# Kernel optimization log

Hardware: AMD Instinct MI355X
Metric: run time of the kernel (lower is better)

Reference implementation:

```python
import jax, jax.numpy as jnp
import numpy as np

N, E, G = 100000, 1600000, 8
IN, H, OUT = 3, 64, 20


def setup_inputs() -> dict:
    key = jax.random.key(0)
    ks = jax.random.split(key, 24)
    def nrm(k, shape, scale=0.1):
        return jax.random.normal(k, shape, dtype=jnp.float32) * scale
    inp = {}
    inp["x"] = jax.random.normal(ks[0], (N, IN), dtype=jnp.float32)
    inp["edge_index"] = jax.random.randint(ks[1], (2, E), 0, N, dtype=jnp.int32)
    inp["batch"] = jnp.sort(jax.random.randint(ks[2], (N,), 0, G, dtype=jnp.int32))
    dims = [(IN, H), (H, H), (H, H)]  # 3 GATConv layers (initial + layers-1)
    for i, (di, do) in enumerate(dims):
        inp[f"W{i}"] = nrm(ks[3 + 4 * i], (di, do))
        inp[f"as{i}"] = nrm(ks[4 + 4 * i], (do,))
        inp[f"ad{i}"] = nrm(ks[5 + 4 * i], (do,))
        inp[f"b{i}"] = jnp.zeros((do,), jnp.float32)
    inp["vn_emb0"] = jnp.zeros((1, H), jnp.float32)  # constant-0 init per module
    inp["m1_w1"] = nrm(ks[15], (H, H)); inp["m1_b1"] = jnp.zeros((H,), jnp.float32)
    inp["m1_w2"] = nrm(ks[16], (H, H)); inp["m1_b2"] = jnp.zeros((H,), jnp.float32)
    inp["mf_w1"] = nrm(ks[17], (H, H)); inp["mf_b1"] = jnp.zeros((H,), jnp.float32)
    inp["mf_w2"] = nrm(ks[18], (H, OUT)); inp["mf_b2"] = jnp.zeros((OUT,), jnp.float32)
    inp["out_w"] = nrm(ks[19], (H, OUT)); inp["out_b"] = jnp.zeros((OUT,), jnp.float32)
    return inp


def _gat(x, src, dst, W, a_s, a_d, b):
    # PyG GATConv, 1 head: h = xW; e_ij = LeakyReLU_0.2(a_s.h_j + a_d.h_i);
    # alpha = softmax over incoming edges of each dst node; out_i = sum_j alpha_ij h_j + b
    h = x @ W                                                  # [N, H]
    lg = jax.nn.leaky_relu((h @ a_s)[src] + (h @ a_d)[dst], 0.2)  # [E+N]
    m = jax.ops.segment_max(lg, dst, num_segments=N)
    m = jnp.where(jnp.isfinite(m), m, 0.0)
    p = jnp.exp(lg - m[dst])
    denom = jax.ops.segment_sum(p, dst, num_segments=N)
    alpha = p / denom[dst]
    return jax.ops.segment_sum(alpha[:, None] * h[src], dst, num_segments=N) + b


def _forward(x, edge_index, batch, params):
    (W0, as0, ad0, b0, W1, as1, ad1, b1, W2, as2, ad2, b2,
     vn_emb0, m1_w1, m1_b1, m1_w2, m1_b2, mf_w1, mf_b1, mf_w2, mf_b2,
     out_w, out_b) = params
    loops = jnp.arange(N, dtype=edge_index.dtype)  # GATConv add_self_loops=True
    src = jnp.concatenate([edge_index[0], loops])
    dst = jnp.concatenate([edge_index[1], loops])
    act = lambda v: jax.nn.leaky_relu(v, 0.01)  # nn.LeakyReLU default slope
    h = act(_gat(x, src, dst, W0, as0, ad0, b0))
    h = act(_gat(h, src, dst, W1, as1, ad1, b1))
    h = act(_gat(h, src, dst, W2, as2, ad2, b2))
    # virtual node: global_add_pool(out, batch) + Embedding(0) (zero-init)
    vn = jax.ops.segment_sum(h, batch, num_segments=G) + vn_emb0[0]
    vn = jax.nn.relu(vn @ m1_w1 + m1_b1)
    vn = jax.nn.relu(vn @ m1_w2 + m1_b2)
    vn = jax.nn.relu(vn @ mf_w1 + mf_b1)
    vn = jax.nn.relu(vn @ mf_w2 + mf_b2)
    return (h @ out_w + out_b, vn)


def reference(x, edge_index, batch, W0, as0, ad0, b0, W1, as1, ad1, b1,
              W2, as2, ad2, b2, vn_emb0, m1_w1, m1_b1, m1_w2, m1_b2,
              mf_w1, mf_b1, mf_w2, mf_b2, out_w, out_b):
    params = (W0, as0, ad0, b0, W1, as1, ad1, b1, W2, as2, ad2, b2,
              vn_emb0, m1_w1, m1_b1, m1_w2, m1_b2, mf_w1, mf_b1, mf_w2, mf_b2,
              out_w, out_b)
    return _forward(x, edge_index, batch, params)
```

## Files before the change

kernel.cpp:

```cpp
#include <hip/hip_runtime.h>
#include <hip/hip_bf16.h>

#define H 64
#define OUTD 20
#define NGRAPH 8
#define CAP 64
#define NBK 256
#define CAPB 8192

typedef __attribute__((ext_vector_type(8))) short bf16x8;
typedef __attribute__((ext_vector_type(4))) float f32x4;
typedef __attribute__((ext_vector_type(8))) unsigned short u16x8;

__device__ __forceinline__ float ldp(const void* p, int i, bool f32) {
    return f32 ? ((const float*)p)[i]
               : __bfloat162float(((const __hip_bfloat16*)p)[i]);
}

__device__ __forceinline__ float bfu(unsigned short u) {
    union { unsigned int i; float f; } c; c.i = ((unsigned)u) << 16; return c.f;
}
__device__ __forceinline__ unsigned short fbits(float f) {
    __hip_bfloat16 b = __float2bfloat16(f);
    return *reinterpret_cast<unsigned short*>(&b);
}

__global__ void detect_dtype(const unsigned short* __restrict__ xb, int n_u16,
                             int* __restrict__ flag) {
    __shared__ int sh[256];
    int t = threadIdx.x;
    int m = min(n_u16, 4096);
    int bad = 0;
    for (int i = t; i < m; i += 256) {
        unsigned e = (xb[i] >> 7) & 0xFF;
        bad += (e >= 0x90) ? 1 : 0;
    }
    sh[t] = bad;
    __syncthreads();
    for (int off = 128; off; off >>= 1) {
        if (t < off) sh[t] += sh[t + off];
        __syncthreads();
    }
    if (t == 0) *flag = (sh[0] > (m >> 4)) ? 1 : 0;
}


__global__ void fillC_dense0(const int* __restrict__ src, const int* __restrict__ dst,
                             int* __restrict__ gcur, unsigned* __restrict__ ebuf,
                             int E, int n, int nC, int EPC, int nbk,
                             const void* __restrict__ x, const void* __restrict__ W,
                             const void* __restrict__ a_s, const void* __restrict__ a_d,
                             __hip_bfloat16* __restrict__ h, float* __restrict__ s,
                             float* __restrict__ d, const int* __restrict__ flagp) {
    if ((int)blockIdx.x < nC) {
        __shared__ unsigned lcnt[NBK];
        __shared__ int lbase[NBK];
        int t = threadIdx.x;
        for (int i = t; i < NBK; i += 256) lcnt[i] = 0;
        __syncthreads();
        int base = blockIdx.x * (256 * EPC) + t;
        for (int i = 0; i < EPC; ++i) {
            int e = base + i * 256;
            if (e < E) {
                int dn = dst[e];
                if ((unsigned)dn < (unsigned)n) atomicAdd(&lcnt[dn >> 9], 1u);
            }
        }
        __syncthreads();
        for (int i = t; i < nbk; i += 256) {
            unsigned c = lcnt[i];
            lbase[i] = c ? atomicAdd(&gcur[i], (int)c) : 0;
            lcnt[i] = 0;
        }
        __syncthreads();
        for (int i = 0; i < EPC; ++i) {
            int e = base + i * 256;
            if (e < E) {
                int dn = dst[e];
                if ((unsigned)dn < (unsigned)n) {
                    int b = dn >> 9;
                    unsigned pos = (unsigned)lbase[b] + atomicAdd(&lcnt[b], 1u);
                    if (pos < CAPB)
                        ebuf[(size_t)b * CAPB + pos] =
                            ((unsigned)src[e] << 9) | (unsigned)(dn & 511);
                }
            }
        }
        return;
    }
    const bool f32 = (*flagp != 0);
    int idx = ((int)blockIdx.x - nC) * 256 + threadIdx.x;
    int node = idx >> 6;
    int f = idx & 63;
    if (node >= n) return;
    float acc = 0.f;
    for (int k = 0; k < 3; ++k)
        acc += ldp(x, node * 3 + k, f32) * ldp(W, k * H + f, f32);
    h[(size_t)node * H + f] = __float2bfloat16(acc);
    float sv = acc * ldp(a_s, f, f32);
    float dv = acc * ldp(a_d, f, f32);
    for (int off = 32; off; off >>= 1) {
        sv += __shfl_xor(sv, off);
        dv += __shfl_xor(dv, off);
    }
    if (f == 0) { s[node] = sv; d[node] = dv; }
}

__global__ __launch_bounds__(512) void bucketD(const unsigned* __restrict__ ebuf,
                                               const int* __restrict__ gcur,
                                               int* __restrict__ cnt,
                                               int* __restrict__ col, int n) {
    __shared__ unsigned lcnt[512];
    int b = blockIdx.x, t = threadIdx.x;
    lcnt[t] = 0;
    __syncthreads();
    int end = min(gcur[b], CAPB);
    const unsigned* reg = ebuf + (size_t)b * CAPB;
    for (int i = t; i < end; i += 512) {
        unsigned e = reg[i];
        int loc = (int)(e & 511u);
        int sn = (int)(e >> 9);
        unsigned pos = atomicAdd(&lcnt[loc], 1u);
        if (pos < CAP) col[(size_t)((b << 9) + loc) * CAP + pos] = sn;
    }
    __syncthreads();
    int node = (b << 9) + t;
    if (node < n) cnt[node] = (int)min(lcnt[t], (unsigned)CAP);
}


__global__ __launch_bounds__(256) void denseN_mfma(
    const __hip_bfloat16* __restrict__ in,
    const void* __restrict__ W,
    const void* __restrict__ a_s, const void* __restrict__ a_d,
    __hip_bfloat16* __restrict__ h, float* __restrict__ s,
    float* __restrict__ d, int n, const int* __restrict__ flagp) {
    const bool f32 = (*flagp != 0);
    __shared__ short Wt[64 * 72];
    int t = threadIdx.x;
    for (int i = t; i < 4096; i += 256) {
        int k = i >> 6, nf = i & 63;
        Wt[nf * 72 + k] = (short)fbits(ldp(W, i, f32));
    }
    __syncthreads();

    int wid = t >> 6, lane = t & 63;
    int quad = lane >> 4, n16 = lane & 15;
    int nodeBase = blockIdx.x * 64 + wid * 16;
    int mrow = nodeBase + n16;
    int mclamp = min(mrow, n - 1);
    const short* inp = (const short*)in;
    const short* arow = inp + (size_t)mclamp * 64;
    bf16x8 a0 = *(const bf16x8*)(arow + quad * 8);
    bf16x8 a1 = *(const bf16x8*)(arow + 32 + quad * 8);

    float as_v[4], ad_v[4];
    for (int nt = 0; nt < 4; ++nt) {
        as_v[nt] = ldp(a_s, nt * 16 + n16, f32);
        ad_v[nt] = ldp(a_d, nt * 16 + n16, f32);
    }

    float sv[4] = {0.f, 0.f, 0.f, 0.f}, dv[4] = {0.f, 0.f, 0.f, 0.f};
    f32x4 accs[4];
    for (int nt = 0; nt < 4; ++nt) {
        const short* wrow = Wt + (nt * 16 + n16) * 72;
        bf16x8 b0 = *(const bf16x8*)(wrow + quad * 8);
        bf16x8 b1 = *(const bf16x8*)(wrow + 32 + quad * 8);
        f32x4 c = {0.f, 0.f, 0.f, 0.f};
        c = __builtin_amdgcn_mfma_f32_16x16x32_bf16(a0, b0, c, 0, 0, 0);
        c = __builtin_amdgcn_mfma_f32_16x16x32_bf16(a1, b1, c, 0, 0, 0);
        accs[nt] = c;
        for (int r = 0; r < 4; ++r) {
            sv[r] += c[r] * as_v[nt];
            dv[r] += c[r] * ad_v[nt];
        }
    }

    for (int r = 0; r < 4; ++r) {
        int node = nodeBase + quad * 4 + r;
        if (node < n) {
            __hip_bfloat16* hr = h + (size_t)node * 64;
            for (int nt = 0; nt < 4; ++nt)
                hr[nt * 16 + n16] = __float2bfloat16(accs[nt][r]);
        }
    }
    for (int r = 0; r < 4; ++r) {
        for (int mask = 1; mask < 16; mask <<= 1) {
            sv[r] += __shfl_xor(sv[r], mask);
            dv[r] += __shfl_xor(dv[r], mask);
        }
    }
    if (n16 == 0) {
        for (int r = 0; r < 4; ++r) {
            int node = nodeBase + quad * 4 + r;
            if (node < n) { s[node] = sv[r]; d[node] = dv[r]; }
        }
    }
}


__global__ void gat_aggregate(const __hip_bfloat16* __restrict__ h,
                              const float* __restrict__ s, const float* __restrict__ d,
                              const int* __restrict__ cnt, const int* __restrict__ col,
                              const void* __restrict__ bias,
                              __hip_bfloat16* __restrict__ out, int n,
                              const int* __restrict__ flagp) {
    const bool f32 = (*flagp != 0);
    int node = (blockIdx.x * blockDim.x + threadIdx.x) >> 6;
    if (node >= n) return;
    int lane = threadIdx.x & 63;
    int deg = min(cnt[node], CAP);
    int D = deg + 1;
    size_t base = (size_t)node * CAP;
    float di = d[node];

    if (D <= 64) {
        bool act = lane < D;
        int j = (lane < deg) ? col[base + lane] : node;
        j = ((unsigned)j < (unsigned)n) ? j : 0;
        float v = act ? s[j] + di : -INFINITY;
        v = v > 0.f ? v : 0.2f * v;
        float m = v;
        for (int off = 32; off; off >>= 1) m = fmaxf(m, __shfl_xor(m, off));
        float wgt = act ? __expf(v - m) : 0.f;
        float wsum = wgt;
        for (int off = 32; off; off >>= 1) wsum += __shfl_xor(wsum, off);

        const u16x8* h8 = (const u16x8*)h;
        int c = lane & 7, q = lane >> 3;
        float a[8] = {0.f, 0.f, 0.f, 0.f, 0.f, 0.f, 0.f, 0.f};
        int groups = (D + 7) >> 3;
        for (int p = 0; p < groups; ++p) {
            int t = 8 * p + q;
            float wt = __shfl(wgt, t);
            int jt = __shfl(j, t);
            u16x8 hv = h8[jt * 8 + c];
            a[0] += wt * bfu(hv[0]);
            a[1] += wt * bfu(hv[1]);
            a[2] += wt * bfu(hv[2]);
            a[3] += wt * bfu(hv[3]);
            a[4] += wt * bfu(hv[4]);
            a[5] += wt * bfu(hv[5]);
            a[6] += wt * bfu(hv[6]);
            a[7] += wt * bfu(hv[7]);
        }
        for (int i = 0; i < 8; ++i) {
            a[i] += __shfl_xor(a[i], 8);
            a[i] += __shfl_xor(a[i], 16);
            a[i] += __shfl_xor(a[i], 32);
        }
        if (lane < 8) {
            float inv = 1.f / fmaxf(wsum, 1e-20f);
            u16x8 ov;
            for (int i = 0; i < 8; ++i) {
                float o = a[i] * inv + ldp(bias, 8 * c + i, f32);
                o = o > 0.f ? o : 0.01f * o;
                ov[i] = fbits(o);
            }
            ((u16x8*)out)[(size_t)node * 8 + c] = ov;
        }
        return;
    }

    float m = -INFINITY;
    for (int e = lane; e < D; e += 64) {
        int j = (e < deg) ? col[base + e] : node;
        j = ((unsigned)j < (unsigned)n) ? j : 0;
        float v = s[j] + di;
        v = v > 0.f ? v : 0.2f * v;
        m = fmaxf(m, v);
    }
    for (int off = 32; off; off >>= 1) m = fmaxf(m, __shfl_xor(m, off));
    if (!(m > -INFINITY)) m = 0.f;

    float acc = 0.f, wsum = 0.f;
    for (int b = 0; b < D; b += 64) {
        int e = b + lane;
        float w = 0.f;
        int j = 0;
        if (e < D) {
            j = (e < deg) ? col[base + e] : node;
            j = ((unsigned)j < (unsigned)n) ? j : 0;
            float v = s[j] + di;
            v = v > 0.f ? v : 0.2f * v;
            w = __expf(v - m);
        }
        wsum += w;
        int c2 = min(64, D - b);
        for (int t = 0; t < c2; ++t) {
            float wt = __shfl(w, t);
            int jt = __shfl(j, t);
            acc += wt * __bfloat162float(h[(size_t)jt * H + lane]);
        }
    }
    for (int off = 32; off; off >>= 1) wsum += __shfl_xor(wsum, off);

    float o = acc / fmaxf(wsum, 1e-20f) + ldp(bias, lane, f32);
    o = o > 0.f ? o : 0.01f * o;
    out[(size_t)node * H + lane] = __float2bfloat16(o);
}


__global__ __launch_bounds__(256) void proj_pool(
    const __hip_bfloat16* __restrict__ h,
    const void* __restrict__ W, const void* __restrict__ b,
    void* __restrict__ out, int n, const int* __restrict__ flagp,
    int projBlocks, const int* __restrict__ batch, float* __restrict__ vn) {
    const bool f32 = (*flagp != 0);
    if ((int)blockIdx.x < projBlocks) {
        __shared__ short Wt[32 * 72];
        int t = threadIdx.x;
        for (int i = t; i < 32 * 64; i += 256) {
            int o = i >> 6, k = i & 63;
            Wt[o * 72 + k] = (o < OUTD) ? (short)fbits(ldp(W, k * OUTD + o, f32)) : 0;
        }
        __syncthreads();

        int wid = t >> 6, lane = t & 63;
        int quad = lane >> 4, n16 = lane & 15;
        int nodeBase = blockIdx.x * 64 + wid * 16;
        int mclamp = min(nodeBase + n16, n - 1);
        const short* arow = (const short*)h + (size_t)mclamp * 64;
        bf16x8 a0 = *(const bf16x8*)(arow + quad * 8);
        bf16x8 a1 = *(const bf16x8*)(arow + 32 + quad * 8);

        f32x4 acc0 = {0.f, 0.f, 0.f, 0.f}, acc1 = {0.f, 0.f, 0.f, 0.f};
        {
            const short* wrow = Wt + n16 * 72;
            bf16x8 b0 = *(const bf16x8*)(wrow + quad * 8);
            bf16x8 b1 = *(const bf16x8*)(wrow + 32 + quad * 8);
            acc0 = __builtin_amdgcn_mfma_f32_16x16x32_bf16(a0, b0, acc0, 0, 0, 0);
            acc0 = __builtin_amdgcn_mfma_f32_16x16x32_bf16(a1, b1, acc0, 0, 0, 0);
        }
        {
            const short* wrow = Wt + (16 + n16) * 72;
            bf16x8 b0 = *(const bf16x8*)(wrow + quad * 8);
            bf16x8 b1 = *(const bf16x8*)(wrow + 32 + quad * 8);
            acc1 = __builtin_amdgcn_mfma_f32_16x16x32_bf16(a0, b0, acc1, 0, 0, 0);
            acc1 = __builtin_amdgcn_mfma_f32_16x16x32_bf16(a1, b1, acc1, 0, 0, 0);
        }
        float bv0 = ldp(b, n16, f32);
        float bv1 = (n16 < OUTD - 16) ? ldp(b, 16 + n16, f32) : 0.f;
        for (int r = 0; r < 4; ++r) {
            int node = nodeBase + quad * 4 + r;
            if (node >= n) break;
            float o0 = acc0[r] + bv0;
            if (f32) ((float*)out)[node * OUTD + n16] = o0;
            else     ((__hip_bfloat16*)out)[node * OUTD + n16] = __float2bfloat16(o0);
            if (n16 < OUTD - 16) {
                float o1 = acc1[r] + bv1;
                if (f32) ((float*)out)[node * OUTD + 16 + n16] = o1;
                else     ((__hip_bfloat16*)out)[node * OUTD + 16 + n16] = __float2bfloat16(o1);
            }
        }
        return;
    }
    __shared__ float part[NGRAPH * H];
    int t = threadIdx.x;
    for (int i = t; i < NGRAPH * H; i += 256) part[i] = 0.f;
    __syncthreads();
    int pb = (int)blockIdx.x - projBlocks;
    int npb = gridDim.x - projBlocks;
    int wid = t >> 6, lane = t & 63;
    int gwave = pb * 4 + wid;
    int nwaves = npb * 4;
    int chunk = (n + nwaves - 1) / nwaves;
    int beg = gwave * chunk;
    int end = min(n, beg + chunk);
    if (beg < end) {
        float acc = 0.f;
        int cur = batch[beg];
        for (int i = beg; i < end; ++i) {
            int g = batch[i];
            if (g != cur) {
                if ((unsigned)cur < NGRAPH) atomicAdd(&part[cur * H + lane], acc);
                acc = 0.f;
                cur = g;
            }
            acc += __bfloat162float(h[(size_t)i * H + lane]);
        }
        if ((unsigned)cur < NGRAPH) atomicAdd(&part[cur * H + lane], acc);
    }
    __syncthreads();
    for (int i = t; i < NGRAPH * H; i += 256) {
        float v = part[i];
        if (v != 0.f) atomicAdd(&vn[i], v);
    }
}


__global__ void vn_mlp(const float* __restrict__ vn, const void* __restrict__ emb,
                       const void* __restrict__ w1, const void* __restrict__ b1,
                       const void* __restrict__ w2, const void* __restrict__ b2,
                       const void* __restrict__ w3, const void* __restrict__ b3,
                       const void* __restrict__ w4, const void* __restrict__ b4,
                       void* __restrict__ out, int out1_off, const int* __restrict__ flagp) {
    const bool f32 = (*flagp != 0);
    __shared__ float A[NGRAPH * H], B[NGRAPH * H];
    int t = threadIdx.x;
    int g = t >> 6, f = t & 63;
    A[t] = vn[t] + ldp(emb, f, f32);
    __syncthreads();
    float acc = ldp(b1, f, f32);
    for (int k = 0; k < H; ++k) acc += A[g * H + k] * ldp(w1, k * H + f, f32);
    B[t] = fmaxf(acc, 0.f);
    __syncthreads();
    acc = ldp(b2, f, f32);
    for (int k = 0; k < H; ++k) acc += B[g * H + k] * ldp(w2, k * H + f, f32);
    A[t] = fmaxf(acc, 0.f);
    __syncthreads();
    acc = ldp(b3, f, f32);
    for (int k = 0; k < H; ++k) acc += A[g * H + k] * ldp(w3, k * H + f, f32);
    B[t] = fmaxf(acc, 0.f);
    __syncthreads();
    if (f < OUTD) {
        acc = ldp(b4, f, f32);
        for (int k = 0; k < H; ++k) acc += B[g * H + k] * ldp(w4, k * OUTD + f, f32);
        acc = fmaxf(acc, 0.f);
        int idx = out1_off + g * OUTD + f;
        if (f32) ((float*)out)[idx] = acc;
        else     ((__hip_bfloat16*)out)[idx] = __float2bfloat16(acc);
    }
}


extern "C" void kernel_launch(void* const* d_in, const int* in_sizes, int n_in,
                              void* d_out, int out_size, void* d_ws, size_t ws_size,
                              hipStream_t stream) {
    const void* x   = d_in[0];
    const int* ei   = (const int*)d_in[1];
    const int* batch= (const int*)d_in[2];
    const void* W0  = d_in[3];
    const void* as0 = d_in[4];
    const void* ad0 = d_in[5];
    const void* b0  = d_in[6];
    const void* W1  = d_in[7];
    const void* as1 = d_in[8];
    const void* ad1 = d_in[9];
    const void* b1  = d_in[10];
    const void* W2  = d_in[11];
    const void* as2 = d_in[12];
    const void* ad2 = d_in[13];
    const void* b2  = d_in[14];
    const void* vne = d_in[15];
    const void* m1w1 = d_in[16];
    const void* m1b1 = d_in[17];
    const void* m1w2 = d_in[18];
    const void* m1b2 = d_in[19];
    const void* mfw1 = d_in[20];
    const void* mfb1 = d_in[21];
    const void* mfw2 = d_in[22];
    const void* mfb2 = d_in[23];
    const void* outw = d_in[24];
    const void* outb = d_in[25];

    const int N = in_sizes[2];
    const int E = in_sizes[1] / 2;
    const int* srcp = ei;
    const int* dstp = ei + E;

    char* w = (char*)d_ws;
    auto alloc = [&](size_t bytes) -> void* {
        void* p = (void*)w;
        w += ((bytes + 255) / 256) * 256;
        return p;
    };
    int*   flag   = (int*)alloc(256);
    int*   gcur   = (int*)alloc((size_t)NBK * 4);
    unsigned* ebuf= (unsigned*)alloc((size_t)NBK * CAPB * 4);
    int*   cnt    = (int*)alloc((size_t)N * 4);
    int*   col    = (int*)alloc((size_t)N * CAP * 4);
    __hip_bfloat16* featA = (__hip_bfloat16*)alloc((size_t)N * H * 2);
    __hip_bfloat16* featB = (__hip_bfloat16*)alloc((size_t)N * H * 2);
    __hip_bfloat16* hbuf  = (__hip_bfloat16*)alloc((size_t)N * H * 2);
    float* sArr   = (float*)alloc((size_t)N * 4);
    float* dArr   = (float*)alloc((size_t)N * 4);
    float* vn     = (float*)alloc((size_t)NGRAPH * H * 4);

    const int nbN64 = (N * H + 255) / 256;
    const int nb64 = (N + 63) / 64;
    const int projBlocks = (N + 63) / 64;
    const int nbk = (N + 511) >> 9;
    int EPC = 32;
    int nC = (E + 256 * EPC - 1) / (256 * EPC);
    while (nC > 256) { EPC <<= 1; nC = (E + 256 * EPC - 1) / (256 * EPC); }

    detect_dtype<<<1, 256, 0, stream>>>((const unsigned short*)x, in_sizes[0], flag);

    hipMemsetAsync(gcur, 0, (size_t)NBK * 4, stream);
    hipMemsetAsync(vn, 0, (size_t)NGRAPH * H * 4, stream);
    fillC_dense0<<<nC + nbN64, 256, 0, stream>>>(
        srcp, dstp, gcur, ebuf, E, N, nC, EPC, nbk,
        x, W0, as0, ad0, hbuf, sArr, dArr, flag);
    bucketD<<<nbk, 512, 0, stream>>>(ebuf, gcur, cnt, col, N);

    gat_aggregate<<<nbN64, 256, 0, stream>>>(hbuf, sArr, dArr, cnt, col, b0, featA, N, flag);
    denseN_mfma<<<nb64, 256, 0, stream>>>(featA, W1, as1, ad1, hbuf, sArr, dArr, N, flag);
    gat_aggregate<<<nbN64, 256, 0, stream>>>(hbuf, sArr, dArr, cnt, col, b1, featB, N, flag);
    denseN_mfma<<<nb64, 256, 0, stream>>>(featB, W2, as2, ad2, hbuf, sArr, dArr, N, flag);
    gat_aggregate<<<nbN64, 256, 0, stream>>>(hbuf, sArr, dArr, cnt, col, b2, featA, N, flag);

    proj_pool<<<projBlocks + 512, 256, 0, stream>>>(featA, outw, outb, d_out, N, flag,
                                                    projBlocks, batch, vn);
    vn_mlp<<<1, 512, 0, stream>>>(vn, vne, m1w1, m1b1, m1w2, m1b2, mfw1, mfb1, mfw2, mfb2,
                                  d_out, N * OUTD, flag);
}
```

Measured before the change: 421.7 us.

## Use compact CSR with packed edge weights and feature-sliced node layout

Replaces the fixed 64-slot per-node adjacency with a compact CSR built by a block prefix scan. Each column entry packs the source index with a 15-bit bf16-truncated attention weight. A separate edge_weights kernel computes the softmax weights per layer. Aggregation then runs over a sliced feature layout ([8 slices][N][8]), so each block gathers one 16-byte slice for a node range, aiming for better cache locality on the random gathers. The cost is an extra kernel per layer and reduced weight precision, and the layout change must stay consistent across all consumers.

After: 549.0 us. 30.2% more time.

```diff
diff --git a/kernel.cpp b/kernel.cpp
--- a/kernel.cpp
+++ b/kernel.cpp
@@ -4,13 +4,14 @@
 #define H 64
 #define OUTD 20
 #define NGRAPH 8
-#define CAP 64
 #define NBK 256
 #define CAPB 8192
+#define MAXDEG 63
 
 typedef __attribute__((ext_vector_type(8))) short bf16x8;
 typedef __attribute__((ext_vector_type(4))) float f32x4;
 typedef __attribute__((ext_vector_type(8))) unsigned short u16x8;
+
 
 __device__ __forceinline__ float ldp(const void* p, int i, bool f32) {
     return f32 ? ((const float*)p)[i]
@@ -96,7 +97,7 @@
     float acc = 0.f;
     for (int k = 0; k < 3; ++k)
         acc += ldp(x, node * 3 + k, f32) * ldp(W, k * H + f, f32);
-    h[(size_t)node * H + f] = __float2bfloat16(acc);
+    ((short*)h)[((size_t)(f >> 3) * n + node) * 8 + (f & 7)] = (short)fbits(acc);
     float sv = acc * ldp(a_s, f, f32);
     float dv = acc * ldp(a_d, f, f32);
     for (int off = 32; off; off >>= 1) {
@@ -109,23 +110,127 @@
 __global__ __launch_bounds__(512) void bucketD(const unsigned* __restrict__ ebuf,
                                                const int* __restrict__ gcur,
                                                int* __restrict__ cnt,
-                                               int* __restrict__ col, int n) {
+                                               int* __restrict__ off,
+                                               unsigned* __restrict__ col,
+                                               int* __restrict__ gtot, int n) {
     __shared__ unsigned lcnt[512];
+    __shared__ int loff[512];
+    __shared__ int sc[512];
+    __shared__ int sdeg[512];
+    __shared__ int sbase;
     int b = blockIdx.x, t = threadIdx.x;
     lcnt[t] = 0;
     __syncthreads();
     int end = min(gcur[b], CAPB);
     const unsigned* reg = ebuf + (size_t)b * CAPB;
+    for (int i = t; i < end; i += 512) atomicAdd(&lcnt[reg[i] & 511u], 1u);
+    __syncthreads();
+    int node = (b << 9) + t;
+    int degc = (node < n) ? (int)min(lcnt[t], (unsigned)MAXDEG) : -1;
+    int slots = degc + 1;
+    sc[t] = slots;
+    __syncthreads();
+    for (int ofs = 1; ofs < 512; ofs <<= 1) {
+        int v = (t >= ofs) ? sc[t - ofs] : 0;
+        __syncthreads();
+        sc[t] += v;
+        __syncthreads();
+    }
+    if (t == 511) sbase = atomicAdd(gtot, sc[511]);
+    __syncthreads();
+    int myoff = sbase + sc[t] - slots;
+    loff[t] = myoff;
+    sdeg[t] = (degc > 0) ? degc : 0;
+    if (node < n) { off[node] = myoff; cnt[node] = (degc > 0) ? degc : 0; }
+    lcnt[t] = 0;
+    __syncthreads();
     for (int i = t; i < end; i += 512) {
         unsigned e = reg[i];
         int loc = (int)(e & 511u);
-        int sn = (int)(e >> 9);
         unsigned pos = atomicAdd(&lcnt[loc], 1u);
-        if (pos < CAP) col[(size_t)((b << 9) + loc) * CAP + pos] = sn;
-    }
-    __syncthreads();
-    int node = (b << 9) + t;
-    if (node < n) cnt[node] = (int)min(lcnt[t], (unsigned)CAP);
+        if ((int)pos < sdeg[loc])
+            col[loff[loc] + pos] = (e >> 9) << 15;
+    }
+}
+
+__global__ void edge_weights(const float* __restrict__ s, const float* __restrict__ d,
+                             const int* __restrict__ cnt, const int* __restrict__ off,
+                             unsigned* __restrict__ col, int n) {
+    int node = ((int)blockIdx.x * 256 + (int)threadIdx.x) >> 6;
+    if (node >= n) return;
+    int lane = threadIdx.x & 63;
+    int deg = cnt[node];
+    int D = deg + 1;
+    int base = off[node];
+    bool act = lane < D;
+    int j = node;
+    if (lane < deg) {
+        unsigned pk = col[base + lane];
+        j = (int)(pk >> 15);
+        j = ((unsigned)j < (unsigned)n) ? j : 0;
+    }
+    float di = d[node];
+    float v = act ? s[j] + di : -INFINITY;
+    v = v > 0.f ? v : 0.2f * v;
+    float m = v;
+    for (int o = 32; o; o >>= 1) m = fmaxf(m, __shfl_xor(m, o));
+    float p = act ? __expf(v - m) : 0.f;
+    float ws = p;
+    for (int o = 32; o; o >>= 1) ws += __shfl_xor(ws, o);
+    if (act) {
+        float alpha = p / fmaxf(ws, 1e-20f);
+        unsigned w15 = ((__float_as_uint(alpha) + 0x8000u) >> 16) & 0x7FFFu;
+        col[base + lane] = ((unsigned)j << 15) | w15;
+    }
+}
+
+__global__ void gat_agg_sliced(const short* __restrict__ hs,
+                               const int* __restrict__ cnt, const int* __restrict__ off,
+                               const unsigned* __restrict__ col,
+                               const void* __restrict__ bias,
+                               short* __restrict__ outs, int n, int halfN,
+                               const int* __restrict__ flagp) {
+    const bool f32 = (*flagp != 0);
+    int shp = (int)blockIdx.x & 7;
+    int sp = shp >> 1, half = shp & 1;
+    int node = half * halfN + ((int)blockIdx.x >> 3) * 16 + ((int)threadIdx.x >> 4);
+    int lim = half ? n : halfN;
+    if (node >= lim) return;
+    int l = threadIdx.x & 15;
+    int c = l & 1, q = l >> 1;
+    int D = cnt[node] + 1;
+    int base = off[node];
+    int slice = 2 * sp + c;
+    const u16x8* h8 = (const u16x8*)hs + (size_t)slice * n;
+    float a[8] = {0.f, 0.f, 0.f, 0.f, 0.f, 0.f, 0.f, 0.f};
+    for (int e = q; e < D; e += 8) {
+        unsigned pk = col[base + e];
+        float wt = __uint_as_float((pk & 0x7FFFu) << 16);
+        u16x8 hv = h8[pk >> 15];
+        a[0] += wt * bfu(hv[0]);
+        a[1] += wt * bfu(hv[1]);
+        a[2] += wt * bfu(hv[2]);
+        a[3] += wt * bfu(hv[3]);
+        a[4] += wt * bfu(hv[4]);
+        a[5] += wt * bfu(hv[5]);
+        a[6] += wt * bfu(hv[6]);
+        a[7] += wt * bfu(hv[7]);
+    }
+#pragma unroll
+    for (int i = 0; i < 8; ++i) {
+        a[i] += __shfl_xor(a[i], 2);
+        a[i] += __shfl_xor(a[i], 4);
+        a[i] += __shfl_xor(a[i], 8);
+    }
+    if (q == 0) {
+        u16x8 ov;
+        for (int i = 0; i < 8; ++i) {
+            float o = a[i] + ldp(bias, slice * 8 + i, f32);
+            o = o > 0.f ? o : 0.01f * o;
+            ov[i] = fbits(o);
+        }
+        *((u16x8*)outs + (size_t)slice * n + node) = ov;
+    }
 }
 
 
@@ -150,9 +255,8 @@
     int mrow = nodeBase + n16;
     int mclamp = min(mrow, n - 1);
     const short* inp = (const short*)in;
-    const short* arow = inp + (size_t)mclamp * 64;
-    bf16x8 a0 = *(const bf16x8*)(arow + quad * 8);
-    bf16x8 a1 = *(const bf16x8*)(arow + 32 + quad * 8);
+    bf16x8 a0 = *(const bf16x8*)(inp + ((size_t)quad * n + mclamp) * 8);
+    bf16x8 a1 = *(const bf16x8*)(inp + ((size_t)(4 + quad) * n + mclamp) * 8);
 
     float as_v[4], ad_v[4];
     for (int nt = 0; nt < 4; ++nt) {
@@ -166,22 +270,24 @@
         const short* wrow = Wt + (nt * 16 + n16) * 72;
         bf16x8 b0 = *(const bf16x8*)(wrow + quad * 8);
         bf16x8 b1 = *(const bf16x8*)(wrow + 32 + quad * 8);
-        f32x4 c = {0.f, 0.f, 0.f, 0.f};
-        c = __builtin_amdgcn_mfma_f32_16x16x32_bf16(a0, b0, c, 0, 0, 0);
-        c = __builtin_amdgcn_mfma_f32_16x16x32_bf16(a1, b1, c, 0, 0, 0);
-        accs[nt] = c;
+        f32x4 cacc = {0.f, 0.f, 0.f, 0.f};
+        cacc = __builtin_amdgcn_mfma_f32_16x16x32_bf16(a0, b0, cacc, 0, 0, 0);
+        cacc = __builtin_amdgcn_mfma_f32_16x16x32_bf16(a1, b1, cacc, 0, 0, 0);
+        accs[nt] = cacc;
         for (int r = 0; r < 4; ++r) {
-            sv[r] += c[r] * as_v[nt];
-            dv[r] += c[r] * ad_v[nt];
-        }
-    }
-
+            sv[r] += cacc[r] * as_v[nt];
+            dv[r] += cacc[r] * ad_v[nt];
+        }
+    }
+
+    short* hb = (short*)h;
     for (int r = 0; r < 4; ++r) {
         int node = nodeBase + quad * 4 + r;
         if (node < n) {
-            __hip_bfloat16* hr = h + (size_t)node * 64;
-            for (int nt = 0; nt < 4; ++nt)
-                hr[nt * 16 + n16] = __float2bfloat16(accs[nt][r]);
+            for (int nt = 0; nt < 4; ++nt) {
+                int f = nt * 16 + n16;
+                hb[((size_t)(f >> 3) * n + node) * 8 + (f & 7)] = (short)fbits(accs[nt][r]);
+            }
         }
     }
     for (int r = 0; r < 4; ++r) {
@@ -196,108 +302,6 @@
             if (node < n) { s[node] = sv[r]; d[node] = dv[r]; }
         }
     }
-}
-
-
-__global__ void gat_aggregate(const __hip_bfloat16* __restrict__ h,
-                              const float* __restrict__ s, const float* __restrict__ d,
-                              const int* __restrict__ cnt, const int* __restrict__ col,
-                              const void* __restrict__ bias,
-                              __hip_bfloat16* __restrict__ out, int n,
-                              const int* __restrict__ flagp) {
-    const bool f32 = (*flagp != 0);
-    int node = (blockIdx.x * blockDim.x + threadIdx.x) >> 6;
-    if (node >= n) return;
-    int lane = threadIdx.x & 63;
-    int deg = min(cnt[node], CAP);
-    int D = deg + 1;
-    size_t base = (size_t)node * CAP;
-    float di = d[node];
-
-    if (D <= 64) {
-        bool act = lane < D;
-        int j = (lane < deg) ? col[base + lane] : node;
-        j = ((unsigned)j < (unsigned)n) ? j : 0;
-        float v = act ? s[j] + di : -INFINITY;
-        v = v > 0.f ? v : 0.2f * v;
-        float m = v;
-        for (int off = 32; off; off >>= 1) m = fmaxf(m, __shfl_xor(m, off));
-        float wgt = act ? __expf(v - m) : 0.f;
-        float wsum = wgt;
-        for (int off = 32; off; off >>= 1) wsum += __shfl_xor(wsum, off);
-
-        const u16x8* h8 = (const u16x8*)h;
-        int c = lane & 7, q = lane >> 3;
-        float a[8] = {0.f, 0.f, 0.f, 0.f, 0.f, 0.f, 0.f, 0.f};
-        int groups = (D + 7) >> 3;
-        for (int p = 0; p < groups; ++p) {
-            int t = 8 * p + q;
-            float wt = __shfl(wgt, t);
-            int jt = __shfl(j, t);
-            u16x8 hv = h8[jt * 8 + c];
-            a[0] += wt * bfu(hv[0]);
-            a[1] += wt * bfu(hv[1]);
-            a[2] += wt * bfu(hv[2]);
-            a[3] += wt * bfu(hv[3]);
-            a[4] += wt * bfu(hv[4]);
-            a[5] += wt * bfu(hv[5]);
-            a[6] += wt * bfu(hv[6]);
-            a[7] += wt * bfu(hv[7]);
-        }
-        for (int i = 0; i < 8; ++i) {
-            a[i] += __shfl_xor(a[i], 8);
-            a[i] += __shfl_xor(a[i], 16);
-            a[i] += __shfl_xor(a[i], 32);
-        }
-        if (lane < 8) {
-            float inv = 1.f / fmaxf(wsum, 1e-20f);
-            u16x8 ov;
-            for (int i = 0; i < 8; ++i) {
-                float o = a[i] * inv + ldp(bias, 8 * c + i, f32);
-                o = o > 0.f ? o : 0.01f * o;
-                ov[i] = fbits(o);
-            }
-            ((u16x8*)out)[(size_t)node * 8 + c] = ov;
-        }
-        return;
-    }
-
-    float m = -INFINITY;
-    for (int e = lane; e < D; e += 64) {
-        int j = (e < deg) ? col[base + e] : node;
-        j = ((unsigned)j < (unsigned)n) ? j : 0;
-        float v = s[j] + di;
-        v = v > 0.f ? v : 0.2f * v;
-        m = fmaxf(m, v);
-    }
-    for (int off = 32; off; off >>= 1) m = fmaxf(m, __shfl_xor(m, off));
-    if (!(m > -INFINITY)) m = 0.f;
-
-    float acc = 0.f, wsum = 0.f;
-    for (int b = 0; b < D; b += 64) {
-        int e = b + lane;
-        float w = 0.f;
-        int j = 0;
-        if (e < D) {
-            j = (e < deg) ? col[base + e] : node;
-            j = ((unsigned)j < (unsigned)n) ? j : 0;
-            float v = s[j] + di;
-            v = v > 0.f ? v : 0.2f * v;
-            w = __expf(v - m);
-        }
-        wsum += w;
-        int c2 = min(64, D - b);
-        for (int t = 0; t < c2; ++t) {
-            float wt = __shfl(w, t);
-            int jt = __shfl(j, t);
-            acc += wt * __bfloat162float(h[(size_t)jt * H + lane]);
-        }
-    }
-    for (int off = 32; off; off >>= 1) wsum += __shfl_xor(wsum, off);
-
-    float o = acc / fmaxf(wsum, 1e-20f) + ldp(bias, lane, f32);
-    o = o > 0.f ? o : 0.01f * o;
-    out[(size_t)node * H + lane] = __float2bfloat16(o);
 }
 
 
@@ -320,9 +324,9 @@
         int quad = lane >> 4, n16 = lane & 15;
         int nodeBase = blockIdx.x * 64 + wid * 16;
         int mclamp = min(nodeBase + n16, n - 1);
-        const short* arow = (const short*)h + (size_t)mclamp * 64;
-        bf16x8 a0 = *(const bf16x8*)(arow + quad * 8);
-        bf16x8 a1 = *(const bf16x8*)(arow + 32 + quad * 8);
+        const short* hsrc = (const short*)h;
+        bf16x8 a0 = *(const bf16x8*)(hsrc + ((size_t)quad * n + mclamp) * 8);
+        bf16x8 a1 = *(const bf16x8*)(hsrc + ((size_t)(4 + quad) * n + mclamp) * 8);
 
         f32x4 acc0 = {0.f, 0.f, 0.f, 0.f}, acc1 = {0.f, 0.f, 0.f, 0.f};
         {
@@ -368,6 +372,7 @@
     int beg = gwave * chunk;
     int end = min(n, beg + chunk);
     if (beg < end) {
+        const short* hb = (const short*)h + (size_t)(lane >> 3) * n * 8 + (lane & 7);
         float acc = 0.f;
         int cur = batch[beg];
         for (int i = beg; i < end; ++i) {
@@ -377,7 +382,7 @@
                 acc = 0.f;
                 cur = g;
             }
-            acc += __bfloat162float(h[(size_t)i * H + lane]);
+            acc += bfu((unsigned short)hb[(size_t)i * 8]);
         }
         if ((unsigned)cur < NGRAPH) atomicAdd(&part[cur * H + lane], acc);
     }
@@ -467,9 +472,11 @@
     };
     int*   flag   = (int*)alloc(256);
     int*   gcur   = (int*)alloc((size_t)NBK * 4);
+    int*   gtot   = (int*)alloc(256);
     unsigned* ebuf= (unsigned*)alloc((size_t)NBK * CAPB * 4);
     int*   cnt    = (int*)alloc((size_t)N * 4);
-    int*   col    = (int*)alloc((size_t)N * CAP * 4);
+    int*   off    = (int*)alloc((size_t)N * 4);
+    unsigned* col = (unsigned*)alloc(((size_t)E + N + 64) * 4);
     __hip_bfloat16* featA = (__hip_bfloat16*)alloc((size_t)N * H * 2);
     __hip_bfloat16* featB = (__hip_bfloat16*)alloc((size_t)N * H * 2);
     __hip_bfloat16* hbuf  = (__hip_bfloat16*)alloc((size_t)N * H * 2);
@@ -481,6 +488,9 @@
     const int nb64 = (N + 63) / 64;
     const int projBlocks = (N + 63) / 64;
     const int nbk = (N + 511) >> 9;
+    const int ewBlocks = (N + 3) / 4;
+    const int halfN = (N + 1) / 2;
+    const int aggBlocks = 8 * ((halfN + 15) / 16);
     int EPC = 32;
     int nC = (E + 256 * EPC - 1) / (256 * EPC);
     while (nC > 256) { EPC <<= 1; nC = (E + 256 * EPC - 1) / (256 * EPC); }
@@ -488,17 +498,24 @@
     detect_dtype<<<1, 256, 0, stream>>>((const unsigned short*)x, in_sizes[0], flag);
 
     hipMemsetAsync(gcur, 0, (size_t)NBK * 4, stream);
+    hipMemsetAsync(gtot, 0, 4, stream);
     hipMemsetAsync(vn, 0, (size_t)NGRAPH * H * 4, stream);
     fillC_dense0<<<nC + nbN64, 256, 0, stream>>>(
         srcp, dstp, gcur, ebuf, E, N, nC, EPC, nbk,
         x, W0, as0, ad0, hbuf, sArr, dArr, flag);
-    bucketD<<<nbk, 512, 0, stream>>>(ebuf, gcur, cnt, col, N);
-
-    gat_aggregate<<<nbN64, 256, 0, stream>>>(hbuf, sArr, dArr, cnt, col, b0, featA, N, flag);
+    bucketD<<<nbk, 512, 0, stream>>>(ebuf, gcur, cnt, off, col, gtot, N);
+
+    edge_weights<<<ewBlocks, 256, 0, stream>>>(sArr, dArr, cnt, off, col, N);
+    gat_agg_sliced<<<aggBlocks, 256, 0, stream>>>((const short*)hbuf, cnt, off, col,
+                                                  b0, (short*)featA, N, halfN, flag);
     denseN_mfma<<<nb64, 256, 0, stream>>>(featA, W1, as1, ad1, hbuf, sArr, dArr, N, flag);
-    gat_aggregate<<<nbN64, 256, 0, stream>>>(hbuf, sArr, dArr, cnt, col, b1, featB, N, flag);
+    edge_weights<<<ewBlocks, 256, 0, stream>>>(sArr, dArr, cnt, off, col, N);
+    gat_agg_sliced<<<aggBlocks, 256, 0, stream>>>((const short*)hbuf, cnt, off, col,
+                                                  b1, (short*)featB, N, halfN, flag);
     denseN_mfma<<<nb64, 256, 0, stream>>>(featB, W2, as2, ad2, hbuf, sArr, dArr, N, flag);
-    gat_aggregate<<<nbN64, 256, 0, stream>>>(hbuf, sArr, dArr, cnt, col, b2, featA, N, flag);
+    edge_weights<<<ewBlocks, 256, 0, stream>>>(sArr, dArr, cnt, off, col, N);
+    gat_agg_sliced<<<aggBlocks, 256, 0, stream>>>((const short*)hbuf, cnt, off, col,
+                                                  b2, (short*)featA, N, halfN, flag);
 
     proj_pool<<<projBlocks + 512, 256, 0, stream>>>(featA, outw, outb, d_out, N, flag,
                                                     projBlocks, batch, vn);
```
